# Optimization experiments

Measured on AMD Instinct MI355X. Metric: run time of the kernel, lower is better.

## Reference

```python
import jax, jax.numpy as jnp
import numpy as np

DIM = 512
NUM_HEADS = 8
HEAD_DIM = DIM // NUM_HEADS
SR = 2
LN_EPS = 1e-5


def setup_inputs() -> dict:
    key = jax.random.key(0)
    ks = jax.random.split(key, 12)
    B, H, W = 8, 32, 32
    N = H * W
    s = 0.02
    return {
        "x": jax.random.normal(ks[0], (B, N, DIM), jnp.float32),
        "H": H,
        "W": W,
        # weights stored as [in, out] (torch Linear applies x @ W.T + b)
        "q_w": jax.random.normal(ks[1], (DIM, DIM), jnp.float32) * s,
        "q_b": jnp.zeros((DIM,), jnp.float32),
        "kv_w": jax.random.normal(ks[2], (DIM, 2 * DIM), jnp.float32) * s,
        "kv_b": jnp.zeros((2 * DIM,), jnp.float32),
        "sr_w": jax.random.normal(ks[3], (DIM, DIM, SR, SR), jnp.float32) * s,  # OIHW
        "sr_b": jnp.zeros((DIM,), jnp.float32),
        "ln_g": jnp.ones((DIM,), jnp.float32),
        "ln_b": jnp.zeros((DIM,), jnp.float32),
        "proj_w": jax.random.normal(ks[4], (DIM, DIM), jnp.float32) * s,
        "proj_b": jnp.zeros((DIM,), jnp.float32),
    }


def reference(x, H, W, q_w, q_b, kv_w, kv_b, sr_w, sr_b, ln_g, ln_b, proj_w, proj_b):
    B, N, C = x.shape
    hd = HEAD_DIM
    scale = hd ** -0.5

    # q: [B, nh, N, hd]
    q = (x @ q_w + q_b).reshape(B, N, NUM_HEADS, hd).transpose(0, 2, 1, 3)

    # spatial reduction conv (stride=kernel=SR) + LayerNorm
    x2d = x.transpose(0, 2, 1).reshape(B, C, H, W)
    x2d = jax.lax.conv_general_dilated(
        x2d, sr_w, window_strides=(SR, SR), padding="VALID",
        dimension_numbers=("NCHW", "OIHW", "NCHW")) + sr_b[None, :, None, None]
    Nk = x2d.shape[2] * x2d.shape[3]
    x_kv = x2d.reshape(B, C, Nk).transpose(0, 2, 1)  # [B, Nk, C]
    mu = x_kv.mean(-1, keepdims=True)
    var = ((x_kv - mu) ** 2).mean(-1, keepdims=True)
    x_kv = (x_kv - mu) * jax.lax.rsqrt(var + LN_EPS) * ln_g + ln_b

    kv = x_kv @ kv_w + kv_b  # [B, Nk, 2C]
    k, v = kv[..., :C], kv[..., C:]
    # Faithful to torch: reshape folds C/hd into kv-sequence axis -> M = Nk*num_heads,
    # shared (broadcast) across all query heads.
    M = Nk * NUM_HEADS
    k = k.reshape(B, M, hd)
    v = v.reshape(B, M, hd)

    attn = jnp.einsum("bhnd,bmd->bhnm", q, k) * scale  # [B, nh, N, M]
    attn = jax.nn.softmax(attn, axis=-1)
    out = jnp.einsum("bhnm,bmd->bhnd", attn, v)  # [B, nh, N, hd]
    out = out.transpose(0, 2, 1, 3).reshape(B, N, C)
    return out @ proj_w + proj_b
```

## Files before the change

### kernel.cpp

```cpp
#include <hip/hip_runtime.h>
#include <hip/hip_bf16.h>
#include <stdint.h>

typedef __attribute__((ext_vector_type(8))) short short8;
typedef __attribute__((ext_vector_type(4))) float f32x4;

#define MFMA(A, B, C) __builtin_amdgcn_mfma_f32_16x16x32_bf16(A, B, C, 0, 0, 0)

__device__ inline uint32_t bfrne(float f) {
  uint32_t u = __float_as_uint(f);
  return (u + 0x7FFFu + ((u >> 16) & 1u)) >> 16;
}

__device__ inline uint32_t pkrne(float a, float b) {
  union { __hip_bfloat162 v; uint32_t u; } c;
  c.v.x = __float2bfloat16(a);
  c.v.y = __float2bfloat16(b);
  return c.u;
}

__device__ inline float fexp2(float x) { return __builtin_amdgcn_exp2f(x); }

__device__ inline void gload16(const short* g, short* l) {
  __builtin_amdgcn_global_load_lds(
      (const __attribute__((address_space(1))) void*)g,
      (__attribute__((address_space(3))) void*)l, 16, 0, 0);
}

__global__ __launch_bounds__(256) void prep_all_kernel(
    const float* __restrict__ sr_w, const float* __restrict__ kv_w,
    const float* __restrict__ q_w, const float* __restrict__ proj_w,
    const float* __restrict__ x,
    short* __restrict__ WcThi, short* __restrict__ kvThi,
    short* __restrict__ qThi, short* __restrict__ pThi,
    short* __restrict__ xhi) {
  __shared__ float tile[32][33];
  const int blk = blockIdx.x;
  if (blk < 4096) {
    int t = blk * 256 + threadIdx.x;
    int kk = t & 2047, o = t >> 11;
    float v = sr_w[(size_t)o * 2048 + ((kk & 511) << 2) + (kk >> 9)];
    WcThi[t] = (short)bfrne(v);
    return;
  }
  if (blk >= 5120) {
    int t = (blk - 5120) * 256 + threadIdx.x;
    float4 v0 = *(const float4*)&x[(size_t)t * 8];
    float4 v1 = *(const float4*)&x[(size_t)t * 8 + 4];
    uint4 pk;
    pk.x = pkrne(v0.x, v0.y);
    pk.y = pkrne(v0.z, v0.w);
    pk.z = pkrne(v1.x, v1.y);
    pk.w = pkrne(v1.z, v1.w);
    *(uint4*)&xhi[(size_t)t * 8] = pk;
    return;
  }
  const float* in; short* ohi; int N, bx, by;
  if (blk < 4608) {
    in = kv_w; ohi = kvThi; N = 1024;
    int i = blk - 4096; bx = i & 31; by = i >> 5;
  } else if (blk < 4864) {
    in = q_w; ohi = qThi; N = 512;
    int i = blk - 4608; bx = i & 15; by = i >> 4;
  } else {
    in = proj_w; ohi = pThi; N = 512;
    int i = blk - 4864; bx = i & 15; by = i >> 4;
  }
  const int K = 512;
  const int tx = threadIdx.x & 31, ty = threadIdx.x >> 5;
#pragma unroll
  for (int i = 0; i < 4; ++i)
    tile[ty + i * 8][tx] = in[(size_t)(by * 32 + ty + i * 8) * N + bx * 32 + tx];
  __syncthreads();
#pragma unroll
  for (int i = 0; i < 4; ++i) {
    int n = bx * 32 + ty + i * 8;
    float v = tile[tx][ty + i * 8];
    ohi[(size_t)n * K + by * 32 + tx] = (short)bfrne(v);
  }
}

__global__ __launch_bounds__(256) void ln_kernel(
    const float* __restrict__ X, const float* __restrict__ g,
    const float* __restrict__ bta, short* __restrict__ hi) {
  const int row = blockIdx.x, t = threadIdx.x;
  size_t idx = (size_t)row * 512 + t * 2;
  const size_t PS = (size_t)2048 * 512;
  float2 a0 = *(const float2*)&X[idx];
  float2 a1 = *(const float2*)&X[idx + PS];
  float2 a2 = *(const float2*)&X[idx + 2 * PS];
  float2 a3 = *(const float2*)&X[idx + 3 * PS];
  float x0 = a0.x + a1.x + a2.x + a3.x;
  float x1 = a0.y + a1.y + a2.y + a3.y;
  float s = x0 + x1, sq = x0 * x0 + x1 * x1;
#pragma unroll
  for (int off = 1; off < 64; off <<= 1) {
    s += __shfl_xor(s, off);
    sq += __shfl_xor(sq, off);
  }
  __shared__ float rs[4], rq[4];
  int wid = t >> 6;
  if ((t & 63) == 0) { rs[wid] = s; rq[wid] = sq; }
  __syncthreads();
  s = rs[0] + rs[1] + rs[2] + rs[3];
  sq = rq[0] + rq[1] + rq[2] + rq[3];
  float mu = s * (1.f / 512), var = sq * (1.f / 512) - mu * mu;
  float inv = rsqrtf(var + 1e-5f);
  float2 gg = *(const float2*)&g[t * 2], bb = *(const float2*)&bta[t * 2];
  float o0 = (x0 - mu) * inv * gg.x + bb.x;
  float o1 = (x1 - mu) * inv * gg.y + bb.y;
  *(uint32_t*)&hi[idx] = pkrne(o0, o1);
}

__global__ void kv_post_kernel(const float* __restrict__ KV1, const float* __restrict__ KV2,
                               short* __restrict__ Kf, short* __restrict__ Vf) {
  const int blk = blockIdx.x;
  if (blk < 4096) {
    int t = blk * 256 + threadIdx.x;
    int j = t & 7, l = (t >> 3) & 63, i = (t >> 9) & 7, tt = (t >> 12) & 31, b = t >> 17;
    int qi = l & 15, g = l >> 4, h2 = i & 1, mf = i >> 1;
    int m = tt * 64 + mf * 16 + qi, d = h2 * 32 + g * 8 + j;
    size_t idx = ((size_t)b * 256 + (m >> 3)) * 1024 + (m & 7) * 64 + d;
    Kf[t] = (short)bfrne(KV1[idx] + KV2[idx]);
  } else {
    int t = (blk - 4096) * 256 + threadIdx.x;
    int j = t & 7, l = (t >> 3) & 63, i = (t >> 9) & 7, tt = (t >> 12) & 31, b = t >> 17;
    int qi = l & 15, g = l >> 4, df = i & 3, ks2 = i >> 2;
    int mm = tt * 64 + ks2 * 32 + g * 8 + j, dd = df * 16 + qi;
    size_t idx = ((size_t)b * 256 + (mm >> 3)) * 1024 + 512 + (mm & 7) * 64 + dd;
    Vf[t] = (short)bfrne(KV1[idx] + KV2[idx]);
  }
}

template <bool GATHER, int OMODE>
__device__ __forceinline__ void gemm_body(
    short* ldsraw,
    const short* __restrict__ Ahi, const short* __restrict__ BThi,
    const float* __restrict__ bias, float* __restrict__ C,
    short* __restrict__ Chi, float oscale,
    int M, int N, int lda, int ldb, int klen,
    int bxx, int byy, int bzz) {
  typedef short (*ldsA_t)[64][8];
  typedef short (*ldsB_t)[128][8];
  ldsA_t ldsA = (ldsA_t)ldsraw;
  ldsB_t ldsB = (ldsB_t)(ldsraw + 4 * 64 * 8);
  const int tid = threadIdx.x, lane = tid & 63, wave = tid >> 6;
  const int g = lane >> 4, qi = lane & 15;
  const int row0 = bxx * 64, col0 = byy * 128;
  const int kz = bzz * klen;
  float* Cz = C + (size_t)bzz * M * N;
  const bool dobias = (bzz == 0);
  f32x4 acc[4][2] = {};
  const int arow = tid & 63, akg = tid >> 6;
  const int bsm = tid & 127, bk2 = (tid >> 7) * 2;

  for (int k0 = kz; k0 < kz + klen; k0 += 32) {
    __syncthreads();
    size_t ao;
    if (GATHER) {
      int row = row0 + arow;
      int bi = row >> 8, p = row & 255;
      int col = k0 + akg * 8;
      int seg = col >> 9, cc = col & 511;
      int n = (2 * (p >> 4) + (seg >> 1)) * 32 + 2 * (p & 15) + (seg & 1);
      ao = ((size_t)bi * 1024 + n) * 512 + cc;
    } else {
      ao = (size_t)(row0 + arow) * lda + k0 + akg * 8;
    }
    gload16(&Ahi[ao], &ldsA[akg][arow][0]);
#pragma unroll
    for (int c = 0; c < 2; ++c) {
      size_t bo = (size_t)(col0 + bsm) * ldb + k0 + (bk2 + c) * 8;
      gload16(&BThi[bo], &ldsB[bk2 + c][bsm][0]);
    }
    __syncthreads();
    short8 ah[4], bh[2];
#pragma unroll
    for (int i = 0; i < 4; ++i)
      ah[i] = *(const short8*)&ldsA[g][i * 16 + qi][0];
#pragma unroll
    for (int j = 0; j < 2; ++j)
      bh[j] = *(const short8*)&ldsB[g][wave * 32 + j * 16 + qi][0];
#pragma unroll
    for (int i = 0; i < 4; ++i)
#pragma unroll
      for (int j = 0; j < 2; ++j)
        acc[i][j] = MFMA(ah[i], bh[j], acc[i][j]);
  }
#pragma unroll
  for (int i = 0; i < 4; ++i)
#pragma unroll
    for (int j = 0; j < 2; ++j) {
      int colb = col0 + wave * 32 + j * 16 + qi;
      float bs = dobias ? bias[colb] : 0.f;
#pragma unroll
      for (int r = 0; r < 4; ++r) {
        int row = row0 + i * 16 + g * 4 + r;
        if (OMODE == 0) {
          Cz[(size_t)row * N + colb] = acc[i][j][r] + bs;
        } else {
          Chi[(size_t)row * N + colb] = (short)bfrne((acc[i][j][r] + bs) * oscale);
        }
      }
    }
}

template <bool GATHER, int OMODE>
__global__ __launch_bounds__(256) void gemm_1p(
    const short* __restrict__ Ahi, const short* __restrict__ BThi,
    const float* __restrict__ bias, float* __restrict__ C,
    short* __restrict__ Chi, float oscale,
    int M, int N, int lda, int ldb, int klen) {
  __shared__ short lds[6144];
  gemm_body<GATHER, OMODE>(lds, Ahi, BThi, bias, C, Chi, oscale,
                           M, N, lda, ldb, klen,
                           blockIdx.x, blockIdx.y, blockIdx.z);
}

__global__ __launch_bounds__(256) void conv_q_kernel(
    const short* __restrict__ xhi, const short* __restrict__ WcThi,
    const float* __restrict__ sr_b, float* __restrict__ Cbuf,
    const short* __restrict__ qThi, const float* __restrict__ q_b,
    short* __restrict__ Qhi, float qscale) {
  __shared__ short lds[6144];
  const int blk = blockIdx.x;
  if (blk < 512) {
    int bx = blk & 31, by = (blk >> 5) & 3, bz = blk >> 7;
    gemm_body<true, 0>(lds, xhi, WcThi, sr_b, Cbuf, nullptr, 1.f,
                       2048, 512, 512, 2048, 512, bx, by, bz);
  } else {
    int i = blk - 512;
    int bx = i & 127, by = i >> 7;
    gemm_body<false, 1>(lds, xhi, qThi, q_b, nullptr, Qhi, qscale,
                        8192, 512, 512, 512, 512, bx, by, 0);
  }
}

__device__ __forceinline__ void ld8(short8 (&dst)[8], const short* base) {
#pragma unroll
  for (int i = 0; i < 8; ++i)
    dst[i] = *(const short8*)&base[(size_t)i * 512];
}

__device__ __forceinline__ void qk_tile(f32x4 (&s)[2][4], const short8 (&kr)[8],
                                        const short8 (&qh)[2][2]) {
  const f32x4 z = {0.f, 0.f, 0.f, 0.f};
  __builtin_amdgcn_s_setprio(1);
#pragma unroll
  for (int mf = 0; mf < 4; ++mf)
#pragma unroll
    for (int qc = 0; qc < 2; ++qc) {
      s[qc][mf] = MFMA(kr[mf * 2 + 0], qh[qc][0], z);
      s[qc][mf] = MFMA(kr[mf * 2 + 1], qh[qc][1], s[qc][mf]);
    }
  __builtin_amdgcn_s_setprio(0);
}

__device__ __forceinline__ void pack_tile(const f32x4 (&s)[2][4], short* Psw,
                                          int g, int qi, int swz) {
#pragma unroll
  for (int qc = 0; qc < 2; ++qc)
#pragma unroll
    for (int mf = 0; mf < 4; ++mf) {
      uint32_t u0 = __float_as_uint(fexp2(s[qc][mf][0]));
      uint32_t u1 = __float_as_uint(fexp2(s[qc][mf][1]));
      uint32_t u2 = __float_as_uint(fexp2(s[qc][mf][2]));
      uint32_t u3 = __float_as_uint(fexp2(s[qc][mf][3]));
      uint2 hp;
      hp.x = (u0 >> 16) | (u1 & 0xffff0000u);
      hp.y = (u2 >> 16) | (u3 & 0xffff0000u);
      int uw = ((mf * 4 + g) ^ swz) << 2;
      *(uint2*)&Psw[qc * 1024 + qi * 64 + uw] = hp;
    }
}

__device__ __forceinline__ void pv_tile(const short8 (&vr)[8], short* Psw,
                                        f32x4 (&lacc)[2], f32x4 (&oacc)[2][4],
                                        int g, int qi, int swz) {
  const short8 ones = {(short)0x3F80, (short)0x3F80, (short)0x3F80, (short)0x3F80,
                       (short)0x3F80, (short)0x3F80, (short)0x3F80, (short)0x3F80};
#pragma unroll
  for (int qc = 0; qc < 2; ++qc)
#pragma unroll
    for (int ks2 = 0; ks2 < 2; ++ks2) {
      int ur = ((ks2 * 8 + g * 2) ^ swz) << 2;
      short8 pa = *(const short8*)&Psw[qc * 1024 + qi * 64 + ur];
      __builtin_amdgcn_s_setprio(1);
      lacc[qc] = MFMA(ones, pa, lacc[qc]);
#pragma unroll
      for (int df = 0; df < 4; ++df)
        oacc[qc][df] = MFMA(vr[ks2 * 4 + df], pa, oacc[qc][df]);
      __builtin_amdgcn_s_setprio(0);
    }
}

__global__ __launch_bounds__(256, 2) void attn_kernel(
    const short* __restrict__ Qhi, const short* __restrict__ Kf,
    const short* __restrict__ Vf, short* __restrict__ Ohi) {
  __shared__ short Ps[4][2][1024];
  const int tid = threadIdx.x, lane = tid & 63, wave = tid >> 6;
  const int g = lane >> 4, qi = lane & 15;
  const int h = blockIdx.y, b = blockIdx.z;
  const int n0 = blockIdx.x * 128 + wave * 32;
  const int swz = (qi & 7) << 1;
  short* Psw = &Ps[wave][0][0];

  short8 qh[2][2];
#pragma unroll
  for (int qc = 0; qc < 2; ++qc) {
    const size_t qrow = ((size_t)b * 1024 + n0 + qc * 16 + qi) * 512 + h * 64;
#pragma unroll
    for (int ks = 0; ks < 2; ++ks)
      qh[qc][ks] = *(const short8*)&Qhi[qrow + (ks * 4 + g) * 8];
  }
  f32x4 lacc[2] = {};
  f32x4 oacc[2][4] = {};
  const short* Kb = Kf + (size_t)b * 131072 + lane * 8;
  const short* Vb = Vf + (size_t)b * 131072 + lane * 8;

  short8 kA[8], kB[8], vr[8];
  f32x4 sA[2][4], sB[2][4];
  ld8(kA, Kb);
  ld8(kB, Kb + 4096);
  qk_tile(sA, kA, qh);
  for (int t = 0; t < 32; t += 2) {
    const short* tK = Kb + (size_t)t * 4096;
    const short* tV = Vb + (size_t)t * 4096;
    ld8(vr, tV);
    if (t < 30) ld8(kA, tK + 8192);
    pack_tile(sA, Psw, g, qi, swz);
    qk_tile(sB, kB, qh);
    pv_tile(vr, Psw, lacc, oacc, g, qi, swz);
    ld8(vr, tV + 4096);
    if (t < 30) ld8(kB, tK + 12288);
    pack_tile(sB, Psw, g, qi, swz);
    if (t < 30) qk_tile(sA, kA, qh);
    pv_tile(vr, Psw, lacc, oacc, g, qi, swz);
  }
#pragma unroll
  for (int qc = 0; qc < 2; ++qc) {
    float linv = 1.f / lacc[qc][0];
    size_t obase = ((size_t)b * 1024 + n0 + qc * 16 + qi) * 512 + h * 64;
#pragma unroll
    for (int df = 0; df < 4; ++df) {
      float o0 = oacc[qc][df][0] * linv, o1 = oacc[qc][df][1] * linv;
      float o2 = oacc[qc][df][2] * linv, o3 = oacc[qc][df][3] * linv;
      uint2 hp;
      hp.x = pkrne(o0, o1);
      hp.y = pkrne(o2, o3);
      *(uint2*)&Ohi[obase + df * 16 + g * 4] = hp;
    }
  }
}

extern "C" void kernel_launch(void* const* d_in, const int* in_sizes, int n_in,
                              void* d_out, int out_size, void* d_ws, size_t ws_size,
                              hipStream_t stream) {
  const float* x      = (const float*)d_in[0];
  const float* q_w    = (const float*)d_in[3];
  const float* q_b    = (const float*)d_in[4];
  const float* kv_w   = (const float*)d_in[5];
  const float* kv_b   = (const float*)d_in[6];
  const float* sr_w   = (const float*)d_in[7];
  const float* sr_b   = (const float*)d_in[8];
  const float* ln_g   = (const float*)d_in[9];
  const float* ln_b   = (const float*)d_in[10];
  const float* proj_w = (const float*)d_in[11];
  const float* proj_b = (const float*)d_in[12];

  char* W = (char*)d_ws;
  const size_t MB = 1024 * 1024;
  short* xhi   = (short*)(W);
  short* WcThi = (short*)(W + 16 * MB);
  float* Cbuf  = (float*)(W + 20 * MB);
  short* LNhi  = (short*)(W + 36 * MB);
  short* kvThi = (short*)(W + 40 * MB);
  short* qThi  = (short*)(W + 42 * MB);
  short* pThi  = (short*)(W + 43 * MB);
  short* Qhi   = (short*)(W + 44 * MB);
  float* KVp   = (float*)(W + 20 * MB);
  short* Kf    = (short*)(W + 36 * MB);
  short* Vf    = (short*)(W + 16 * MB);
  short* Ohi   = (short*)(W);

  prep_all_kernel<<<7168, 256, 0, stream>>>(
      sr_w, kv_w, q_w, proj_w, x, WcThi, kvThi, qThi, pThi, xhi);
  conv_q_kernel<<<1024, 256, 0, stream>>>(
      xhi, WcThi, sr_b, Cbuf, qThi, q_b, Qhi, 0.125f * 1.44269504f);
  ln_kernel<<<2048, 256, 0, stream>>>(Cbuf, ln_g, ln_b, LNhi);
  gemm_1p<false, 0><<<dim3(32, 8, 2), 256, 0, stream>>>(
      LNhi, kvThi, kv_b, KVp, nullptr, 1.f, 2048, 1024, 512, 512, 256);
  kv_post_kernel<<<8192, 256, 0, stream>>>(KVp, KVp + (size_t)2 * MB, Kf, Vf);
  attn_kernel<<<dim3(8, 8, 8), 256, 0, stream>>>(Qhi, Kf, Vf, Ohi);
  gemm_1p<false, 0><<<dim3(128, 4, 1), 256, 0, stream>>>(
      Ohi, pThi, proj_b, (float*)d_out, nullptr, 1.f, 8192, 512, 512, 512, 512);
}
```

Measured before the change: 128.2 us.

## Split attention KV sequence in two and combine partial outputs

Splits the key/value sequence of the attention kernel into two halves processed by separate blocks, doubling the grid from 512 to 1024 blocks and raising the occupancy hint. Each half writes a normalized bf16 partial output plus its row sum, and a new combine kernel merges them with weights based on those row sums. This targets low occupancy across the GPU's compute units, at the cost of an extra launch, extra global traffic, and an added bf16 rounding step. The combine relies on the softmax having no running max, which matches how the existing kernel already works.

```diff
diff --git a/kernel.cpp b/kernel.cpp
--- a/kernel.cpp
+++ b/kernel.cpp
@@ -20,6 +20,10 @@
 }
 
 __device__ inline float fexp2(float x) { return __builtin_amdgcn_exp2f(x); }
+
+__device__ inline float bf2f(short h) {
+  return __uint_as_float(((uint32_t)(uint16_t)h) << 16);
+}
 
 __device__ inline void gload16(const short* g, short* l) {
   __builtin_amdgcn_global_load_lds(
@@ -294,13 +298,14 @@
     }
 }
 
-__global__ __launch_bounds__(256, 2) void attn_kernel(
+__global__ __launch_bounds__(256, 4) void attn_kernel(
     const short* __restrict__ Qhi, const short* __restrict__ Kf,
-    const short* __restrict__ Vf, short* __restrict__ Ohi) {
+    const short* __restrict__ Vf, short* __restrict__ Opart, float* __restrict__ Lbuf) {
   __shared__ short Ps[4][2][1024];
   const int tid = threadIdx.x, lane = tid & 63, wave = tid >> 6;
   const int g = lane >> 4, qi = lane & 15;
-  const int h = blockIdx.y, b = blockIdx.z;
+  const int h = blockIdx.y;
+  const int b = blockIdx.z & 7, split = blockIdx.z >> 3;
   const int n0 = blockIdx.x * 128 + wave * 32;
   const int swz = (qi & 7) << 1;
   short* Psw = &Ps[wave][0][0];
@@ -315,32 +320,36 @@
   }
   f32x4 lacc[2] = {};
   f32x4 oacc[2][4] = {};
-  const short* Kb = Kf + (size_t)b * 131072 + lane * 8;
-  const short* Vb = Vf + (size_t)b * 131072 + lane * 8;
+  const short* Kb = Kf + (size_t)b * 131072 + (size_t)split * 65536 + lane * 8;
+  const short* Vb = Vf + (size_t)b * 131072 + (size_t)split * 65536 + lane * 8;
 
   short8 kA[8], kB[8], vr[8];
   f32x4 sA[2][4], sB[2][4];
   ld8(kA, Kb);
   ld8(kB, Kb + 4096);
   qk_tile(sA, kA, qh);
-  for (int t = 0; t < 32; t += 2) {
+  for (int t = 0; t < 16; t += 2) {
     const short* tK = Kb + (size_t)t * 4096;
     const short* tV = Vb + (size_t)t * 4096;
     ld8(vr, tV);
-    if (t < 30) ld8(kA, tK + 8192);
+    if (t < 14) ld8(kA, tK + 8192);
     pack_tile(sA, Psw, g, qi, swz);
     qk_tile(sB, kB, qh);
     pv_tile(vr, Psw, lacc, oacc, g, qi, swz);
     ld8(vr, tV + 4096);
-    if (t < 30) ld8(kB, tK + 12288);
+    if (t < 14) ld8(kB, tK + 12288);
     pack_tile(sB, Psw, g, qi, swz);
-    if (t < 30) qk_tile(sA, kA, qh);
+    if (t < 14) qk_tile(sA, kA, qh);
     pv_tile(vr, Psw, lacc, oacc, g, qi, swz);
   }
+  short* OP = Opart + (size_t)split * (8u * 1024 * 512);
 #pragma unroll
   for (int qc = 0; qc < 2; ++qc) {
-    float linv = 1.f / lacc[qc][0];
-    size_t obase = ((size_t)b * 1024 + n0 + qc * 16 + qi) * 512 + h * 64;
+    float l = lacc[qc][0];
+    float linv = 1.f / l;
+    int q = n0 + qc * 16 + qi;
+    if (g == 0) Lbuf[((size_t)split * 64 + b * 8 + h) * 1024 + q] = l;
+    size_t obase = ((size_t)b * 1024 + q) * 512 + h * 64;
 #pragma unroll
     for (int df = 0; df < 4; ++df) {
       float o0 = oacc[qc][df][0] * linv, o1 = oacc[qc][df][1] * linv;
@@ -348,9 +357,35 @@
       uint2 hp;
       hp.x = pkrne(o0, o1);
       hp.y = pkrne(o2, o3);
-      *(uint2*)&Ohi[obase + df * 16 + g * 4] = hp;
-    }
-  }
+      *(uint2*)&OP[obase + df * 16 + g * 4] = hp;
+    }
+  }
+}
+
+__global__ void combine_kernel(const short* __restrict__ Op, const float* __restrict__ L,
+                               short* __restrict__ Ohi) {
+  const size_t PART = (size_t)8 * 1024 * 512;
+  int c = blockIdx.x * 256 + threadIdx.x;
+  size_t off = (size_t)c * 8;
+  int row = (int)(off >> 9);
+  int b = row >> 10, q = row & 1023;
+  int h = (int)((off & 511) >> 6);
+  float L1 = L[((size_t)b * 8 + h) * 1024 + q];
+  float L2 = L[((size_t)64 + b * 8 + h) * 1024 + q];
+  float w1 = L1 / (L1 + L2);
+  float w2 = 1.f - w1;
+  short8 o1 = *(const short8*)&Op[off];
+  short8 o2 = *(const short8*)&Op[PART + off];
+  float v[8];
+#pragma unroll
+  for (int j = 0; j < 8; ++j)
+    v[j] = bf2f(o1[j]) * w1 + bf2f(o2[j]) * w2;
+  uint4 pk;
+  pk.x = pkrne(v[0], v[1]);
+  pk.y = pkrne(v[2], v[3]);
+  pk.z = pkrne(v[4], v[5]);
+  pk.w = pkrne(v[6], v[7]);
+  *(uint4*)&Ohi[off] = pk;
 }
 
 extern "C" void kernel_launch(void* const* d_in, const int* in_sizes, int n_in,
@@ -381,6 +416,8 @@
   float* KVp   = (float*)(W + 20 * MB);
   short* Kf    = (short*)(W + 36 * MB);
   short* Vf    = (short*)(W + 16 * MB);
+  float* Lbuf  = (float*)(W + 18 * MB);
+  short* Opart = (short*)(W + 20 * MB);
   short* Ohi   = (short*)(W);
 
   prep_all_kernel<<<7168, 256, 0, stream>>>(
@@ -391,7 +428,8 @@
   gemm_1p<false, 0><<<dim3(32, 8, 2), 256, 0, stream>>>(
       LNhi, kvThi, kv_b, KVp, nullptr, 1.f, 2048, 1024, 512, 512, 256);
   kv_post_kernel<<<8192, 256, 0, stream>>>(KVp, KVp + (size_t)2 * MB, Kf, Vf);
-  attn_kernel<<<dim3(8, 8, 8), 256, 0, stream>>>(Qhi, Kf, Vf, Ohi);
+  attn_kernel<<<dim3(8, 8, 16), 256, 0, stream>>>(Qhi, Kf, Vf, Opart, Lbuf);
+  combine_kernel<<<2048, 256, 0, stream>>>(Opart, Lbuf, Ohi);
   gemm_1p<false, 0><<<dim3(128, 4, 1), 256, 0, stream>>>(
       Ohi, pThi, proj_b, (float*)d_out, nullptr, 1.f, 8192, 512, 512, 512, 512);
 }
```

After: 391.6 us. 205% more time.
